# Optimization experiments

Measured on AMD Instinct MI355X. Metric: run time of the kernel, lower is better.

Reference implementation:

```python
import jax, jax.numpy as jnp
import numpy as np

NUM_USERS = 1_000_000
NUM_CANDS = 500_000
EMB_DIM = 32
BATCH = 1024
TOP_K = 10


def setup_inputs() -> dict:
    key = jax.random.key(0)
    k1, k2, k3 = jax.random.split(key, 3)
    user_ids = jax.random.randint(k1, (BATCH,), 0, NUM_USERS, dtype=jnp.int64 if jax.config.jax_enable_x64 else jnp.int32)
    user_table = jax.random.normal(k2, (NUM_USERS, EMB_DIM), dtype=jnp.float32)
    cand_table = jax.random.normal(k3, (NUM_CANDS, EMB_DIM), dtype=jnp.float32)
    return {"user_ids": user_ids, "user_table": user_table, "cand_table": cand_table}


def reference(user_ids, user_table, cand_table):
    # Embedding lookup: [B, D]
    user_embeddings = user_table[user_ids]
    # Brute-force dot-product scoring vs all candidates: [B, C]
    scores = jnp.einsum("bd,cd->bc", user_embeddings, cand_table)
    # Top-k retrieval, return_scores=False -> indices only: [B, K]
    _, top_indices = jax.lax.top_k(scores, TOP_K)
    return user_embeddings, top_indices
```

## Files before the change

kernel.cpp:

```cpp
#include <hip/hip_runtime.h>
#include <hip/hip_bf16.h>
#include <cstdint>
#include <cstddef>

#define BATCH  1024
#define NCANDS 500000
#define DIM    32
#define TOPK   10

#define CAP    1024
#define T_Z    3.55f
#define DELTA  0.2f

#define NCHF   512
#define CPBF   992

#define NCHF3  992
#define CPBF3  512

using bf16x8 = __attribute__((ext_vector_type(8))) short;
using f32x4  = __attribute__((ext_vector_type(4))) float;
using u32x4  = __attribute__((ext_vector_type(4))) unsigned int;

__device__ __forceinline__ unsigned int fau(float f) { return __float_as_uint(f); }
__device__ __forceinline__ float uaf(unsigned int u) { return __uint_as_float(u); }

__device__ __forceinline__ void split3(const float* __restrict__ p,
                                       bf16x8& H, bf16x8& M, bf16x8& L) {
  float4 f0 = ((const float4*)p)[0];
  float4 f1 = ((const float4*)p)[1];
  float f[8] = {f0.x, f0.y, f0.z, f0.w, f1.x, f1.y, f1.z, f1.w};
  unsigned int hp[4], mp[4], lp[4];
#pragma unroll
  for (int q = 0; q < 4; ++q) {
    float a = f[2*q], b = f[2*q+1];
    unsigned int ba = fau(a), bb = fau(b);
    unsigned int ha = ba & 0xFFFF0000u, hb = bb & 0xFFFF0000u;
    hp[q] = (ba >> 16) | hb;
    float ea = a - uaf(ha), eb = b - uaf(hb);
    unsigned int mea = fau(ea) & 0xFFFF0000u, meb = fau(eb) & 0xFFFF0000u;
    mp[q] = (fau(ea) >> 16) | meb;
    float la = ea - uaf(mea), lb = eb - uaf(meb);
    lp[q] = (fau(la) >> 16) | (fau(lb) & 0xFFFF0000u);
  }
  u32x4 hv = {hp[0], hp[1], hp[2], hp[3]};
  u32x4 mv = {mp[0], mp[1], mp[2], mp[3]};
  u32x4 lv = {lp[0], lp[1], lp[2], lp[3]};
  H = __builtin_bit_cast(bf16x8, hv);
  M = __builtin_bit_cast(bf16x8, mv);
  L = __builtin_bit_cast(bf16x8, lv);
}

__device__ __forceinline__ unsigned int rne1(float x) {
  unsigned int b = fau(x);
  return (b + 0x7FFFu + ((b >> 16) & 1u)) >> 16;
}
__device__ __forceinline__ bf16x8 rne8(float4 a, float4 b) {
  u32x4 v = { rne1(a.x) | (rne1(a.y) << 16),
              rne1(a.z) | (rne1(a.w) << 16),
              rne1(b.x) | (rne1(b.y) << 16),
              rne1(b.z) | (rne1(b.w) << 16) };
  return __builtin_bit_cast(bf16x8, v);
}

__global__ __launch_bounds__(256) void pack_kernel(const float* __restrict__ cand,
                                                   short* __restrict__ cb) {
  const int n = NCANDS * DIM / 8;
  for (int i = blockIdx.x * 256 + threadIdx.x; i < n; i += gridDim.x * 256) {
    const float4* p = (const float4*)(cand + (size_t)i * 8);
    float4 a = p[0], b = p[1];
    ((bf16x8*)cb)[i] = rne8(a, b);
  }
}

__global__ __launch_bounds__(256) void prep_kernel(
    const int* __restrict__ ids, const float* __restrict__ ut,
    float* __restrict__ ue, float* __restrict__ Tu,
    float* __restrict__ Tmin4, int* __restrict__ cnt)
{
  int u = blockIdx.x * 256 + threadIdx.x;
  const float4* src = (const float4*)(ut + (size_t)ids[u] * DIM);
  float4* dst = (float4*)(ue + (size_t)u * DIM);
  float n2 = 0.f;
#pragma unroll
  for (int q = 0; q < 8; ++q) {
    float4 v = src[q];
    dst[q] = v;
    n2 += v.x * v.x + v.y * v.y + v.z * v.z + v.w * v.w;
  }
  float t = T_Z * sqrtf(n2) - DELTA;
  Tu[u] = t;
  cnt[u] = 0;
  float t1 = __shfl_xor(t, 1, 64); t = fminf(t, t1);
  float t2 = __shfl_xor(t, 2, 64); t = fminf(t, t2);
  if ((threadIdx.x & 3) == 0) Tmin4[u >> 2] = t;
}

__global__ __launch_bounds__(1024, 4) void filter_kernel_lds(
    const float* __restrict__ ue, const short* __restrict__ cb,
    const float* __restrict__ Tu,
    int* __restrict__ cnt, int* __restrict__ surv)
{
  __shared__ int4 Bs[CPBF3 * 4];

  const int tid  = threadIdx.x;
  const int wave = tid >> 6;
  const int lane = tid & 63;
  const int col  = lane & 15;
  const int quad = lane >> 4;
  const int ch   = blockIdx.x;
  const int ubase = wave * 64;
  const int c0base = ch * CPBF3;

  {
    const int4* gsrc = (const int4*)cb;
#pragma unroll
    for (int it = 0; it < 2; ++it) {
      int i = it * 1024 + tid;
      int row = c0base + (i >> 2);
      int rc = row < NCANDS ? row : 0;
      Bs[i] = gsrc[(size_t)rc * 4 + (i & 3)];
    }
  }

  bf16x8 AH[4];
  float  TuR[4][4];
  float  Tm[4];
#pragma unroll
  for (int g = 0; g < 4; ++g) {
    const float4* ap = (const float4*)(ue + (size_t)(ubase + g * 16 + col) * DIM + quad * 8);
    AH[g] = rne8(ap[0], ap[1]);
#pragma unroll
    for (int r = 0; r < 4; ++r)
      TuR[g][r] = Tu[ubase + g * 16 + quad * 4 + r];
    Tm[g] = fminf(fminf(TuR[g][0], TuR[g][1]), fminf(TuR[g][2], TuR[g][3]));
  }
  const float TmW = fminf(fminf(Tm[0], Tm[1]), fminf(Tm[2], Tm[3]));

  __syncthreads();

#pragma unroll 2
  for (int t = 0; t < (CPBF3 >> 4); ++t) {
    const int r_loc  = (t << 4) + col;
    const int brow_c = c0base + r_loc;
    const bool valid = (brow_c < NCANDS);

    bf16x8 B = __builtin_bit_cast(bf16x8, Bs[r_loc * 4 + quad]);

    f32x4 acc[4];
#pragma unroll
    for (int g = 0; g < 4; ++g) {
      f32x4 z = {0.f, 0.f, 0.f, 0.f};
      acc[g] = __builtin_amdgcn_mfma_f32_16x16x32_bf16(AH[g], B, z, 0, 0, 0);
    }

    float mg[4];
#pragma unroll
    for (int g = 0; g < 4; ++g)
      mg[g] = fmaxf(fmaxf(acc[g][0], acc[g][1]), fmaxf(acc[g][2], acc[g][3]));
    const float mm = fmaxf(fmaxf(mg[0], mg[1]), fmaxf(mg[2], mg[3]));

    if (__ballot(valid && (mm >= TmW))) {
#pragma unroll
      for (int g = 0; g < 4; ++g) {
        if (__ballot(valid && (mg[g] >= Tm[g]))) {
#pragma unroll
          for (int r = 0; r < 4; ++r) {
            if (valid && acc[g][r] >= TuR[g][r]) {
              int u = ubase + g * 16 + quad * 4 + r;
              int pos = atomicAdd(cnt + u, 1);
              if (pos < CAP) surv[(size_t)u * CAP + pos] = brow_c;
            }
          }
        }
      }
    }
  }
}

__global__ __launch_bounds__(256, 4) void filter_kernel_f32(
    const float* __restrict__ ue, const float* __restrict__ cand,
    const float* __restrict__ Tu, const float* __restrict__ Tmin4,
    int* __restrict__ cnt, int* __restrict__ surv)
{
  const int tid  = threadIdx.x;
  const int wave = tid >> 6;
  const int lane = tid & 63;
  const int col  = lane & 15;
  const int quad = lane >> 4;
  const int ub   = blockIdx.x & 1;
  const int ch   = blockIdx.x >> 1;
  const int ubase = ub * 512 + wave * 128;

  bf16x8 AH[8];
  float  Tm[8];
#pragma unroll
  for (int g = 0; g < 8; ++g) {
    const float4* ap = (const float4*)(ue + (size_t)(ubase + g * 16 + col) * DIM + quad * 8);
    AH[g] = rne8(ap[0], ap[1]);
    Tm[g] = Tmin4[(ubase >> 2) + g * 4 + quad];
  }

  const int c0base = ch * CPBF;
  for (int t = 0; t < (CPBF >> 4); ++t) {
    const int brow = c0base + (t << 4) + col;
    const bool valid = (brow < NCANDS);
    const int brc = valid ? brow : 0;
    const float4* bp = (const float4*)(cand + (size_t)brc * DIM + quad * 8);
    float4 b0 = bp[0], b1 = bp[1];
    bf16x8 BH = rne8(b0, b1);

    f32x4 acc[8];
#pragma unroll
    for (int g = 0; g < 8; ++g) {
      f32x4 z = {0.f, 0.f, 0.f, 0.f};
      acc[g] = __builtin_amdgcn_mfma_f32_16x16x32_bf16(AH[g], BH, z, 0, 0, 0);
    }

#pragma unroll
    for (int g = 0; g < 8; ++g) {
      float m = fmaxf(fmaxf(acc[g][0], acc[g][1]), fmaxf(acc[g][2], acc[g][3]));
      if (__ballot(valid && (m >= Tm[g]))) {
#pragma unroll
        for (int r = 0; r < 4; ++r) {
          int u = ubase + g * 16 + quad * 4 + r;
          if (valid && acc[g][r] >= Tu[u]) {
            int pos = atomicAdd(cnt + u, 1);
            if (pos < CAP) surv[(size_t)u * CAP + pos] = brow;
          }
        }
      }
    }
  }
}

__global__ __launch_bounds__(256) void select_kernel(
    const float* __restrict__ ue, const float* __restrict__ cand,
    const int* __restrict__ cnt, const int* __restrict__ surv,
    float* __restrict__ outIdx)
{
  const int wave = threadIdx.x >> 6;
  const int lane = threadIdx.x & 63;
  const int col  = lane & 15;
  const int quad = lane >> 4;
  const int u    = blockIdx.x * 4 + wave;

  bf16x8 AH, AM, AL;
  split3(ue + (size_t)u * DIM + quad * 8, AH, AM, AL);

  int n = cnt[u];
  if (n > CAP) n = CAP;

  float ls[TOPK]; int li[TOPK];
#pragma unroll
  for (int j = 0; j < TOPK; ++j) { ls[j] = -INFINITY; li[j] = 0x7FFFFFFF; }

  const int ntile = (n + 15) >> 4;
  for (int t = 0; t < ntile; ++t) {
    int j = (t << 4) + col;
    bool jv = (j < n);
    int c = jv ? surv[(size_t)u * CAP + j] : 0;

    bf16x8 BH, BM, BL;
    split3(cand + (size_t)c * DIM + quad * 8, BH, BM, BL);

    f32x4 acc = {0.f, 0.f, 0.f, 0.f};
    acc = __builtin_amdgcn_mfma_f32_16x16x32_bf16(AH, BH, acc, 0, 0, 0);
    acc = __builtin_amdgcn_mfma_f32_16x16x32_bf16(AM, BH, acc, 0, 0, 0);
    acc = __builtin_amdgcn_mfma_f32_16x16x32_bf16(AH, BM, acc, 0, 0, 0);
    acc = __builtin_amdgcn_mfma_f32_16x16x32_bf16(AL, BH, acc, 0, 0, 0);
    acc = __builtin_amdgcn_mfma_f32_16x16x32_bf16(AH, BL, acc, 0, 0, 0);
    acc = __builtin_amdgcn_mfma_f32_16x16x32_bf16(AM, BM, acc, 0, 0, 0);

    float s = acc[0];
    if (quad == 0 && jv) {
      if (s > ls[TOPK - 1] || (s == ls[TOPK - 1] && c < li[TOPK - 1])) {
        float cs = s; int ci = c;
#pragma unroll
        for (int j2 = 0; j2 < TOPK; ++j2) {
          if (cs > ls[j2] || (cs == ls[j2] && ci < li[j2])) {
            float tf = ls[j2]; ls[j2] = cs; cs = tf;
            int   tt = li[j2]; li[j2] = ci; ci = tt;
          }
        }
      }
    }
  }

  for (int k = 0; k < TOPK; ++k) {
    float b = ls[0]; int bi = li[0]; int bl = lane;
#pragma unroll
    for (int off = 1; off <= 8; off <<= 1) {
      float ob = __shfl_xor(b, off, 64);
      int   oi = __shfl_xor(bi, off, 64);
      int   ol = __shfl_xor(bl, off, 64);
      bool take = (ob > b) || (ob == b && (oi < bi || (oi == bi && ol < bl)));
      if (take) { b = ob; bi = oi; bl = ol; }
    }
    if (lane == 0) outIdx[(size_t)u * TOPK + k] = (float)bi;
    if (lane == bl) {
#pragma unroll
      for (int j = 0; j < TOPK - 1; ++j) { ls[j] = ls[j + 1]; li[j] = li[j + 1]; }
      ls[TOPK - 1] = -INFINITY; li[TOPK - 1] = 0x7FFFFFFF;
    }
  }
}

__global__ void gather_kernel(const int* __restrict__ ids,
                              const float* __restrict__ ut,
                              float* __restrict__ ue) {
  int i = blockIdx.x * blockDim.x + threadIdx.x;
  if (i < BATCH * DIM) {
    int b = i >> 5, d = i & 31;
    ue[i] = ut[(size_t)ids[b] * DIM + d];
  }
}

__global__ __launch_bounds__(256) void score_topk_fallback(
    const float* __restrict__ ue,
    const float* __restrict__ cand,
    float* __restrict__ ps, int* __restrict__ pi,
    int nchunk, int cpb)
{
  const int tid  = threadIdx.x;
  const int wave = tid >> 6;
  const int lane = tid & 63;
  const int col  = lane & 15;
  const int quad = lane >> 4;
  const int ub   = blockIdx.x & 15;
  const int ch   = blockIdx.x >> 4;
  const int ubase = ub * 64 + wave * 16;

  bf16x8 AH, AM, AL;
  split3(ue + (size_t)(ubase + col) * DIM + quad * 8, AH, AM, AL);

  float ts[4][TOPK];
  int   ti[4][TOPK];
#pragma unroll
  for (int r = 0; r < 4; ++r)
#pragma unroll
    for (int j = 0; j < TOPK; ++j) { ts[r][j] = -INFINITY; ti[r][j] = 0; }

  const int c_start = ch * cpb;
  const int ntiles  = cpb >> 4;
  for (int t = 0; t < ntiles; ++t) {
    int c0   = c_start + (t << 4);
    int brow = c0 + col;
    bool valid = (brow < NCANDS);
    int brc = valid ? brow : (NCANDS - 1);

    bf16x8 BH, BM, BL;
    split3(cand + (size_t)brc * DIM + quad * 8, BH, BM, BL);

    f32x4 acc = {0.f, 0.f, 0.f, 0.f};
    acc = __builtin_amdgcn_mfma_f32_16x16x32_bf16(AH, BH, acc, 0, 0, 0);
    acc = __builtin_amdgcn_mfma_f32_16x16x32_bf16(AM, BH, acc, 0, 0, 0);
    acc = __builtin_amdgcn_mfma_f32_16x16x32_bf16(AH, BM, acc, 0, 0, 0);
    acc = __builtin_amdgcn_mfma_f32_16x16x32_bf16(AL, BH, acc, 0, 0, 0);
    acc = __builtin_amdgcn_mfma_f32_16x16x32_bf16(AH, BL, acc, 0, 0, 0);
    acc = __builtin_amdgcn_mfma_f32_16x16x32_bf16(AM, BM, acc, 0, 0, 0);

#pragma unroll
    for (int r = 0; r < 4; ++r) {
      float s = acc[r];
      if (valid && s > ts[r][TOPK - 1]) {
        float cs = s; int ci = brow;
#pragma unroll
        for (int j = 0; j < TOPK; ++j) {
          if (cs > ts[r][j]) {
            float tf = ts[r][j]; ts[r][j] = cs; cs = tf;
            int   tt = ti[r][j]; ti[r][j] = ci; ci = tt;
          }
        }
      }
    }
  }

#pragma unroll
  for (int r = 0; r < 4; ++r) {
    int u = ubase + quad * 4 + r;
    size_t base = ((size_t)(u * nchunk + ch) * 16 + col) * TOPK;
#pragma unroll
    for (int j = 0; j < TOPK; ++j) { ps[base + j] = ts[r][j]; pi[base + j] = ti[r][j]; }
  }
}

__global__ __launch_bounds__(256) void merge_kernel(
    const float* __restrict__ ps, const int* __restrict__ pi,
    float* __restrict__ out, int E)
{
  const int wave = threadIdx.x >> 6;
  const int lane = threadIdx.x & 63;
  const int u    = blockIdx.x * 4 + wave;

  float lsv[TOPK]; int liv[TOPK];
#pragma unroll
  for (int j = 0; j < TOPK; ++j) { lsv[j] = -INFINITY; liv[j] = 0x7FFFFFFF; }

  size_t base = (size_t)u * E;
  for (int e = lane; e < E; e += 64) {
    float s = ps[base + e];
    int   i = pi[base + e];
    if (s > lsv[TOPK - 1]) {
      float cs = s; int ci = i;
#pragma unroll
      for (int j = 0; j < TOPK; ++j) {
        if (cs > lsv[j] || (cs == lsv[j] && ci < liv[j])) {
          float tf = lsv[j]; lsv[j] = cs; cs = tf;
          int   tt = liv[j]; liv[j] = ci; ci = tt;
        }
      }
    }
  }

  for (int k = 0; k < TOPK; ++k) {
    float b = lsv[0]; int bi = liv[0]; int bl = lane;
#pragma unroll
    for (int off = 32; off > 0; off >>= 1) {
      float ob = __shfl_xor(b, off, 64);
      int   oi = __shfl_xor(bi, off, 64);
      int   ol = __shfl_xor(bl, off, 64);
      bool take = (ob > b) || (ob == b && (oi < bi || (oi == bi && ol < bl)));
      if (take) { b = ob; bi = oi; bl = ol; }
    }
    if (lane == 0) out[(size_t)u * TOPK + k] = (float)bi;
    if (lane == bl) {
#pragma unroll
      for (int j = 0; j < TOPK - 1; ++j) { lsv[j] = lsv[j + 1]; liv[j] = liv[j + 1]; }
      lsv[TOPK - 1] = -INFINITY; liv[TOPK - 1] = 0x7FFFFFFF;
    }
  }
}

extern "C" void kernel_launch(void* const* d_in, const int* in_sizes, int n_in,
                              void* d_out, int out_size, void* d_ws, size_t ws_size,
                              hipStream_t stream) {
  const int*   ids  = (const int*)d_in[0];
  const float* ut   = (const float*)d_in[1];
  const float* cand = (const float*)d_in[2];

  float* ue     = (float*)d_out;
  float* outIdx = ue + BATCH * DIM;

  const size_t base_need = BATCH * 4  + (BATCH / 4) * 4  +
                           BATCH * 4  + (size_t)BATCH * CAP * 4  + 256;
  const size_t pack_bytes = (size_t)NCANDS * DIM * 2;
  const size_t pack_need  = base_need + pack_bytes + 256;

  if (ws_size >= base_need) {
    char* p = (char*)d_ws;
    float* Tu    = (float*)p;  p += BATCH * 4;
    float* Tmin4 = (float*)p;  p += (BATCH / 4) * 4;
    int*   cnt   = (int*)p;    p += BATCH * 4;
    int*   surv  = (int*)p;    p += (size_t)BATCH * CAP * 4;

    hipLaunchKernelGGL(prep_kernel, dim3(BATCH / 256), dim3(256), 0, stream,
                       ids, ut, ue, Tu, Tmin4, cnt);

    if (ws_size >= pack_need) {
      short* cb = (short*)p;
      hipLaunchKernelGGL(pack_kernel, dim3(2048), dim3(256), 0, stream, cand, cb);
      hipLaunchKernelGGL(filter_kernel_lds, dim3(NCHF3), dim3(1024), 0, stream,
                         ue, cb, Tu, cnt, surv);
    } else {
      hipLaunchKernelGGL(filter_kernel_f32, dim3(2 * NCHF), dim3(256), 0, stream,
                         ue, cand, Tu, Tmin4, cnt, surv);
    }

    hipLaunchKernelGGL(select_kernel, dim3(BATCH / 4), dim3(256), 0, stream,
                       ue, cand, cnt, surv, outIdx);
  } else {
    hipLaunchKernelGGL(gather_kernel, dim3((BATCH * DIM + 255) / 256), dim3(256), 0, stream,
                       ids, ut, ue);
    int nchunk = 32;
    while (nchunk > 1 && (size_t)nchunk * BATCH * (16 * TOPK) * 8 > ws_size) nchunk >>= 1;
    int cpb = ((NCANDS + nchunk - 1) / nchunk + 15) & ~15;
    size_t total = (size_t)BATCH * nchunk * 16 * TOPK;
    float* ps = (float*)d_ws;
    int*   pi = (int*)((char*)d_ws + total * sizeof(float));
    hipLaunchKernelGGL(score_topk_fallback, dim3(nchunk * 16), dim3(256), 0, stream,
                       ue, cand, ps, pi, nchunk, cpb);
    hipLaunchKernelGGL(merge_kernel, dim3(BATCH / 4), dim3(256), 0, stream,
                       ps, pi, outIdx, nchunk * 16 * TOPK);
  }
}
```

Before: 323.6 us.

## Fuse bf16 packing into filter kernel with double-buffered LDS chunks

Removes the separate pack kernel that converted the candidate table to bf16 in workspace. The filter kernel now loads fp32 candidate rows straight from global memory, rounds them to bf16 and writes them into a double-buffered LDS tile. Each block processes four 512-row chunks and prefetches the next chunk while scoring the current one. This avoids the extra global write and re-read of the packed table and one kernel launch, but the grid shrinks to 248 blocks and each block reads twice as many bytes from the fp32 source.

```diff
diff --git a/kernel.cpp b/kernel.cpp
--- a/kernel.cpp
+++ b/kernel.cpp
@@ -15,8 +15,9 @@
 #define NCHF   512
 #define CPBF   992
 
-#define NCHF3  992
-#define CPBF3  512
+#define CROWS  512
+#define CHPB   4
+#define NBLKF  248
 
 using bf16x8 = __attribute__((ext_vector_type(8))) short;
 using f32x4  = __attribute__((ext_vector_type(4))) float;
@@ -63,16 +64,6 @@
   return __builtin_bit_cast(bf16x8, v);
 }
 
-__global__ __launch_bounds__(256) void pack_kernel(const float* __restrict__ cand,
-                                                   short* __restrict__ cb) {
-  const int n = NCANDS * DIM / 8;
-  for (int i = blockIdx.x * 256 + threadIdx.x; i < n; i += gridDim.x * 256) {
-    const float4* p = (const float4*)(cand + (size_t)i * 8);
-    float4 a = p[0], b = p[1];
-    ((bf16x8*)cb)[i] = rne8(a, b);
-  }
-}
-
 __global__ __launch_bounds__(256) void prep_kernel(
     const int* __restrict__ ids, const float* __restrict__ ut,
     float* __restrict__ ue, float* __restrict__ Tu,
@@ -96,32 +87,20 @@
   if ((threadIdx.x & 3) == 0) Tmin4[u >> 2] = t;
 }
 
-__global__ __launch_bounds__(1024, 4) void filter_kernel_lds(
-    const float* __restrict__ ue, const short* __restrict__ cb,
+__global__ __launch_bounds__(1024, 4) void filter_kernel_fused(
+    const float* __restrict__ ue, const float* __restrict__ cand,
     const float* __restrict__ Tu,
     int* __restrict__ cnt, int* __restrict__ surv)
 {
-  __shared__ int4 Bs[CPBF3 * 4];
+  __shared__ int4 Bs[2][CROWS * 4];
 
   const int tid  = threadIdx.x;
   const int wave = tid >> 6;
   const int lane = tid & 63;
   const int col  = lane & 15;
   const int quad = lane >> 4;
-  const int ch   = blockIdx.x;
-  const int ubase = wave * 64;
-  const int c0base = ch * CPBF3;
-
-  {
-    const int4* gsrc = (const int4*)cb;
-#pragma unroll
-    for (int it = 0; it < 2; ++it) {
-      int i = it * 1024 + tid;
-      int row = c0base + (i >> 2);
-      int rc = row < NCANDS ? row : 0;
-      Bs[i] = gsrc[(size_t)rc * 4 + (i & 3)];
-    }
-  }
+  const int chunk0 = blockIdx.x * CHPB;
+  const int ubase  = wave * 64;
 
   bf16x8 AH[4];
   float  TuR[4][4];
@@ -137,45 +116,80 @@
   }
   const float TmW = fminf(fminf(Tm[0], Tm[1]), fminf(Tm[2], Tm[3]));
 
+  float4 sa0, sb0, sa1, sb1;
+
+  const int i0 = tid, i1 = 1024 + tid;
+  const int lr0 = i0 >> 2, q0 = i0 & 3;
+  const int lr1 = i1 >> 2, q1 = i1 & 3;
+
+#define STAGE_LOAD(c0)                                                        \
+  {                                                                           \
+    int r0 = (c0) + lr0; r0 = r0 < NCANDS ? r0 : NCANDS - 1;                  \
+    int r1 = (c0) + lr1; r1 = r1 < NCANDS ? r1 : NCANDS - 1;                  \
+    const float4* p0 = (const float4*)(cand + (size_t)r0 * DIM + q0 * 8);     \
+    const float4* p1 = (const float4*)(cand + (size_t)r1 * DIM + q1 * 8);     \
+    sa0 = p0[0]; sb0 = p0[1];                                                 \
+    sa1 = p1[0]; sb1 = p1[1];                                                 \
+  }
+#define STAGE_WRITE(buf)                                                      \
+  {                                                                           \
+    Bs[buf][i0] = __builtin_bit_cast(int4, rne8(sa0, sb0));                   \
+    Bs[buf][i1] = __builtin_bit_cast(int4, rne8(sa1, sb1));                   \
+  }
+
+  STAGE_LOAD(chunk0 * CROWS);
+  STAGE_WRITE(0);
   __syncthreads();
 
+  int cur = 0;
+  for (int c = 0; c < CHPB; ++c) {
+    const int c0base = (chunk0 + c) * CROWS;
+    const bool havenext = (c + 1 < CHPB);
+    if (havenext) STAGE_LOAD((chunk0 + c + 1) * CROWS);
+
+    int nt = (NCANDS - c0base) >> 4;
+    nt = nt < 0 ? 0 : (nt > (CROWS >> 4) ? (CROWS >> 4) : nt);
+
 #pragma unroll 2
-  for (int t = 0; t < (CPBF3 >> 4); ++t) {
-    const int r_loc  = (t << 4) + col;
-    const int brow_c = c0base + r_loc;
-    const bool valid = (brow_c < NCANDS);
-
-    bf16x8 B = __builtin_bit_cast(bf16x8, Bs[r_loc * 4 + quad]);
-
-    f32x4 acc[4];
-#pragma unroll
-    for (int g = 0; g < 4; ++g) {
-      f32x4 z = {0.f, 0.f, 0.f, 0.f};
-      acc[g] = __builtin_amdgcn_mfma_f32_16x16x32_bf16(AH[g], B, z, 0, 0, 0);
-    }
-
-    float mg[4];
-#pragma unroll
-    for (int g = 0; g < 4; ++g)
-      mg[g] = fmaxf(fmaxf(acc[g][0], acc[g][1]), fmaxf(acc[g][2], acc[g][3]));
-    const float mm = fmaxf(fmaxf(mg[0], mg[1]), fmaxf(mg[2], mg[3]));
-
-    if (__ballot(valid && (mm >= TmW))) {
+    for (int t = 0; t < nt; ++t) {
+      bf16x8 B = __builtin_bit_cast(bf16x8, Bs[cur][t * 64 + col * 4 + quad]);
+
+      f32x4 acc[4];
 #pragma unroll
       for (int g = 0; g < 4; ++g) {
-        if (__ballot(valid && (mg[g] >= Tm[g]))) {
-#pragma unroll
-          for (int r = 0; r < 4; ++r) {
-            if (valid && acc[g][r] >= TuR[g][r]) {
-              int u = ubase + g * 16 + quad * 4 + r;
-              int pos = atomicAdd(cnt + u, 1);
-              if (pos < CAP) surv[(size_t)u * CAP + pos] = brow_c;
+        f32x4 z = {0.f, 0.f, 0.f, 0.f};
+        acc[g] = __builtin_amdgcn_mfma_f32_16x16x32_bf16(AH[g], B, z, 0, 0, 0);
+      }
+
+      float mg[4];
+#pragma unroll
+      for (int g = 0; g < 4; ++g)
+        mg[g] = fmaxf(fmaxf(fmaxf(acc[g][0], acc[g][1]), acc[g][2]), acc[g][3]);
+      const float mm = fmaxf(fmaxf(fmaxf(mg[0], mg[1]), mg[2]), mg[3]);
+
+      if (__ballot(mm >= TmW)) {
+#pragma unroll
+        for (int g = 0; g < 4; ++g) {
+          if (__ballot(mg[g] >= Tm[g])) {
+#pragma unroll
+            for (int r = 0; r < 4; ++r) {
+              if (acc[g][r] >= TuR[g][r]) {
+                int u = ubase + g * 16 + quad * 4 + r;
+                int pos = atomicAdd(cnt + u, 1);
+                if (pos < CAP) surv[(size_t)u * CAP + pos] = c0base + (t << 4) + col;
+              }
             }
           }
         }
       }
     }
-  }
+
+    if (havenext) STAGE_WRITE(cur ^ 1);
+    __syncthreads();
+    cur ^= 1;
+  }
+#undef STAGE_LOAD
+#undef STAGE_WRITE
 }
 
 __global__ __launch_bounds__(256, 4) void filter_kernel_f32(
@@ -444,8 +458,6 @@
 
   const size_t base_need = BATCH * 4  + (BATCH / 4) * 4  +
                            BATCH * 4  + (size_t)BATCH * CAP * 4  + 256;
-  const size_t pack_bytes = (size_t)NCANDS * DIM * 2;
-  const size_t pack_need  = base_need + pack_bytes + 256;
 
   if (ws_size >= base_need) {
     char* p = (char*)d_ws;
@@ -456,17 +468,8 @@
 
     hipLaunchKernelGGL(prep_kernel, dim3(BATCH / 256), dim3(256), 0, stream,
                        ids, ut, ue, Tu, Tmin4, cnt);
-
-    if (ws_size >= pack_need) {
-      short* cb = (short*)p;
-      hipLaunchKernelGGL(pack_kernel, dim3(2048), dim3(256), 0, stream, cand, cb);
-      hipLaunchKernelGGL(filter_kernel_lds, dim3(NCHF3), dim3(1024), 0, stream,
-                         ue, cb, Tu, cnt, surv);
-    } else {
-      hipLaunchKernelGGL(filter_kernel_f32, dim3(2 * NCHF), dim3(256), 0, stream,
-                         ue, cand, Tu, Tmin4, cnt, surv);
-    }
-
+    hipLaunchKernelGGL(filter_kernel_fused, dim3(NBLKF), dim3(1024), 0, stream,
+                       ue, cand, Tu, cnt, surv);
     hipLaunchKernelGGL(select_kernel, dim3(BATCH / 4), dim3(256), 0, stream,
                        ue, cand, cnt, surv, outIdx);
   } else {
```

Result: faster. 296.6 us (-8.4%).
